# Performance work log

Hardware: AMD Instinct MI355X
Metric: run time of the kernel (lower is better)

## Reference

```python
import jax, jax.numpy as jnp
import numpy as np

CHUNK, STEP, NCHUNK = 75, 25, 22
DIM, HEADS = 64, 8
BN_EPS = 1e-5


def _conv1d(x, w, b):
    # x: [N, Cin, L], w: [Cout, Cin, K] (torch layout), VALID padding, stride 1
    y = jax.lax.conv_general_dilated(x, w, (1,), 'VALID',
                                     dimension_numbers=('NCH', 'OIH', 'NCH'))
    return y + b[None, :, None]


def _bn(x, gamma, beta, mean, var):
    # inference-mode batchnorm over channel dim of [N, C, L]
    scale = gamma / jnp.sqrt(var + BN_EPS)
    return (x - mean[None, :, None]) * scale[None, :, None] + beta[None, :, None]


def _swish(x):
    return x * jax.nn.sigmoid(x)


def _encode(audio, p):
    # audio: [B, 1, L] -> overlapping chunks [B, 22, 1, 75] via gather (unfold)
    B = audio.shape[0]
    idx = np.arange(NCHUNK)[:, None] * STEP + np.arange(CHUNK)[None, :]  # [22, 75]
    x = audio[:, :, idx]                      # [B, 1, 22, 75]
    x = x.transpose(0, 2, 1, 3).reshape(B * NCHUNK, 1, CHUNK)
    x = _swish(_bn(_conv1d(x, p['w1'], p['b1']), p['g1'], p['be1'], p['m1'], p['v1']))  # [B*22,16,50]
    x = _swish(_bn(_conv1d(x, p['w2'], p['b2']), p['g2'], p['be2'], p['m2'], p['v2']))  # [B*22,32,25]
    x = _swish(_bn(_conv1d(x, p['w3'], p['b3']), p['g3'], p['be3'], p['m3'], p['v3']))  # [B*22,64,1]
    return x[:, :, 0].reshape(B, NCHUNK, DIM)  # concat over chunks == seq of 22 tokens


def _mha(feat, p):
    # per-head full-width linears (torch Linear: y = x @ W.T + b), stacked over heads
    # Wq/Wk/Wv: [H, D, D]; bq/bk/bv: [H, D]
    B, S, D = feat.shape
    Q = jnp.einsum('bsd,hed->bhse', feat, p['Wq']) + p['bq'][None, :, None, :]
    K = jnp.einsum('bsd,hed->bhse', feat, p['Wk']) + p['bk'][None, :, None, :]
    V = jnp.einsum('bsd,hed->bhse', feat, p['Wv']) + p['bv'][None, :, None, :]
    A = jax.nn.softmax(jnp.einsum('bhse,bhte->bhst', Q, K), axis=-1)  # no 1/sqrt(d) scaling in source
    O = jnp.einsum('bhst,bhte->bhse', A, V)       # [B, H, S, D]
    O = O.transpose(0, 2, 1, 3).reshape(B, S, HEADS * D)  # concat heads along feature dim
    return O @ p['Wfc'].T + p['bfc']              # [B, S, D]


def setup_inputs() -> dict:
    key = jax.random.key(0)
    ks = jax.random.split(key, 16)
    B, L = 4096, 600
    C1, C2 = DIM // 4, DIM // 2
    inp = {
        'audio_vec1': jax.random.normal(ks[0], (B, 1, L), jnp.float32),
        'audio_vec2': jax.random.normal(ks[1], (B, 1, L), jnp.float32),
        # conv stack
        'w1': jax.random.normal(ks[2], (C1, 1, 26), jnp.float32) * 0.05,
        'b1': jnp.zeros((C1,), jnp.float32),
        'g1': jnp.ones((C1,), jnp.float32), 'be1': jnp.zeros((C1,), jnp.float32),
        'm1': jnp.zeros((C1,), jnp.float32), 'v1': jnp.ones((C1,), jnp.float32),
        'w2': jax.random.normal(ks[3], (C2, C1, 26), jnp.float32) * 0.05,
        'b2': jnp.zeros((C2,), jnp.float32),
        'g2': jnp.ones((C2,), jnp.float32), 'be2': jnp.zeros((C2,), jnp.float32),
        'm2': jnp.zeros((C2,), jnp.float32), 'v2': jnp.ones((C2,), jnp.float32),
        'w3': jax.random.normal(ks[4], (DIM, C2, 25), jnp.float32) * 0.05,
        'b3': jnp.zeros((DIM,), jnp.float32),
        'g3': jnp.ones((DIM,), jnp.float32), 'be3': jnp.zeros((DIM,), jnp.float32),
        'm3': jnp.zeros((DIM,), jnp.float32), 'v3': jnp.ones((DIM,), jnp.float32),
        # attention (per-head full-width projections)
        'Wq': jax.random.normal(ks[5], (HEADS, DIM, DIM), jnp.float32) * 0.05,
        'bq': jnp.zeros((HEADS, DIM), jnp.float32),
        'Wk': jax.random.normal(ks[6], (HEADS, DIM, DIM), jnp.float32) * 0.05,
        'bk': jnp.zeros((HEADS, DIM), jnp.float32),
        'Wv': jax.random.normal(ks[7], (HEADS, DIM, DIM), jnp.float32) * 0.05,
        'bv': jnp.zeros((HEADS, DIM), jnp.float32),
        'Wfc': jax.random.normal(ks[8], (DIM, HEADS * DIM), jnp.float32) * 0.05,
        'bfc': jnp.zeros((DIM,), jnp.float32),
        # final fc
        'Wout': jax.random.normal(ks[9], (DIM, DIM), jnp.float32) * 0.05,
        'bout': jnp.zeros((DIM,), jnp.float32),
    }
    return inp


def reference(audio_vec1, audio_vec2, w1, b1, g1, be1, m1, v1,
              w2, b2, g2, be2, m2, v2, w3, b3, g3, be3, m3, v3,
              Wq, bq, Wk, bk, Wv, bv, Wfc, bfc, Wout, bout):
    p = dict(w1=w1, b1=b1, g1=g1, be1=be1, m1=m1, v1=v1,
             w2=w2, b2=b2, g2=g2, be2=be2, m2=m2, v2=v2,
             w3=w3, b3=b3, g3=g3, be3=be3, m3=m3, v3=v3,
             Wq=Wq, bq=bq, Wk=Wk, bk=bk, Wv=Wv, bv=bv, Wfc=Wfc, bfc=bfc)
    f1 = _encode(audio_vec1, p)   # [B, 22, 64]
    f2 = _encode(audio_vec2, p)
    f1 = _mha(f1, p).mean(axis=1) @ Wout.T + bout  # [B, 64]
    f2 = _mha(f2, p).mean(axis=1) @ Wout.T + bout
    return (f1, f2)
```

## Files before the change

### kernel.cpp

```cpp
#include <hip/hip_runtime.h>
#include <math.h>

#define NCHUNK 22
#define SEQLEN 600
#define BN_EPS 1e-5f

#define OFF_W1F    0
#define OFF_W2F    1024
#define OFF_W3F    14336
#define OFF_MHF    65536
#define OFF_WC     98304
#define OFF_UH     131072
#define OFF_WH     131584
#define OFF_CH     132096
#define OFF_CBIAS  132104
#define OFF_WCOMB  132168
#define OFF_FEAT   164936
#define REPACK_N   132104

typedef short bf16x8 __attribute__((ext_vector_type(8)));
typedef float f32x4 __attribute__((ext_vector_type(4)));
typedef float f32x16 __attribute__((ext_vector_type(16)));

#if __has_builtin(__builtin_amdgcn_perm)
#define PERM_HI(r0, r1) __builtin_amdgcn_perm((r1), (r0), 0x05040100u)
#define PERM_LO(r0, r1) __builtin_amdgcn_perm((r1), (r0), 0x07060302u)
#else
#define PERM_HI(r0, r1) (((r0) & 0xFFFFu) | ((r1) << 16))
#define PERM_LO(r0, r1) (((r0) >> 16) | ((r1) & 0xFFFF0000u))
#endif

__device__ __forceinline__ float swishf(float z) {
    return z / (1.f + __expf(-z));
}
__device__ __forceinline__ unsigned short bf16_rne(float f) {
    unsigned int u = __float_as_uint(f);
    return (unsigned short)((u + 0x7FFFu + ((u >> 16) & 1u)) >> 16);
}
__device__ __forceinline__ float bf16_tof(unsigned short h) {
    return __uint_as_float(((unsigned int)h) << 16);
}
__device__ __forceinline__ unsigned int pack_hl(float f) {
    unsigned int u = __float_as_uint(f);
    unsigned int h = (u + 0x7FFFu + ((u >> 16) & 1u)) >> 16;
    float r = f - __uint_as_float(h << 16);
    unsigned int v = __float_as_uint(r);
    unsigned int l = (v + 0x7FFFu + ((v >> 16) & 1u)) >> 16;
    return h | (l << 16);
}
__device__ __forceinline__ unsigned int dup_word(float f, int pat) {
    unsigned short h = bf16_rne(f);
    unsigned short v = pat ? bf16_rne(f - bf16_tof(h)) : h;
    return (unsigned int)v | ((unsigned int)v << 16);
}
__device__ __forceinline__ unsigned int frag_word(float f0, float f1, int hl) {
    unsigned short h0 = bf16_rne(f0), h1 = bf16_rne(f1);
    if (hl == 0) return (unsigned int)h0 | ((unsigned int)h1 << 16);
    unsigned short l0 = bf16_rne(f0 - bf16_tof(h0));
    unsigned short l1 = bf16_rne(f1 - bf16_tof(h1));
    return (unsigned int)l0 | ((unsigned int)l1 << 16);
}
__device__ __forceinline__ void frag_from_packed(const unsigned int* p, bf16x8& h8, bf16x8& l8) {
    unsigned int r0 = p[0], r1 = p[1], r2 = p[2], r3 = p[3];
    unsigned int r4 = p[4], r5 = p[5], r6 = p[6], r7 = p[7];
    union U { unsigned int w[4]; bf16x8 v; } H, L;
    H.w[0] = PERM_HI(r0, r1); H.w[1] = PERM_HI(r2, r3);
    H.w[2] = PERM_HI(r4, r5); H.w[3] = PERM_HI(r6, r7);
    L.w[0] = PERM_LO(r0, r1); L.w[1] = PERM_LO(r2, r3);
    L.w[2] = PERM_LO(r4, r5); L.w[3] = PERM_LO(r6, r7);
    h8 = H.v; l8 = L.v;
}

__global__ __launch_bounds__(256) void repack_kernel(
    const float* __restrict__ w1, const float* __restrict__ w2, const float* __restrict__ w3,
    const float* __restrict__ Wq, const float* __restrict__ Wk, const float* __restrict__ Wv,
    const float* __restrict__ Wfc, const float* __restrict__ Wout,
    const float* __restrict__ bq, const float* __restrict__ bk,
    float* __restrict__ ws)
{
    int tid = blockIdx.x * 256 + threadIdx.x;
    unsigned int* wsu = (unsigned int*)ws;
    if (tid < 1024) {
        int r = tid & 3, lane = (tid >> 2) & 63, pat = (tid >> 8) & 1, ph = (tid >> 9) & 1;
        int li = lane & 15, lg = lane >> 4;
        int k = ph * 16 + lg * 4 + r;
        float f = (k < 26) ? w1[li * 26 + k] : 0.f;
        wsu[OFF_W1F + tid] = dup_word(f, pat);
    }
    int t2 = tid - 1024;
    if (t2 >= 0 && t2 < 13312) {
        int r = t2 & 3, lane = (t2 >> 2) & 63, hl = (t2 >> 8) & 1, s = t2 >> 9;
        int co = lane & 31;
        int ci0 = (lane >> 5) * 8;
        float f0 = w2[co * 416 + (ci0 + 2 * r) * 26 + s];
        float f1 = w2[co * 416 + (ci0 + 2 * r + 1) * 26 + s];
        wsu[OFF_W2F + t2] = frag_word(f0, f1, hl);
    }
    int t3 = tid - 14336;
    if (t3 >= 0 && t3 < 51200) {
        int r = t3 & 3, l = (t3 >> 2) & 63, hl = (t3 >> 8) & 1;
        int nt = (t3 >> 9) & 3, s = t3 >> 11;
        int co = nt * 16 + (l & 15);
        int k0 = s * 32 + (l >> 4) * 8 + 2 * r;
        float f0 = w3[co * 800 + (k0 & 31) * 25 + (k0 >> 5)];
        float f1 = w3[co * 800 + ((k0 + 1) & 31) * 25 + ((k0 + 1) >> 5)];
        wsu[OFF_W3F + t3] = frag_word(f0, f1, hl);
    }
    int t4 = tid - 65536;
    if (t4 >= 0 && t4 < 32768) {
        int r = t4 & 3, l = (t4 >> 2) & 63, hl = (t4 >> 8) & 1;
        int nt = (t4 >> 9) & 3, ks = (t4 >> 11) & 1, h = t4 >> 12;
        int n = nt * 16 + (l & 15);
        int d0 = ks * 32 + (l >> 4) * 8 + 2 * r;
        const float* wqh = Wq + h * 4096;
        const float* wkh = Wk + h * 4096;
        float f0 = 0.f, f1 = 0.f;
        #pragma unroll 8
        for (int e = 0; e < 64; ++e) {
            float wk_en = wkh[e * 64 + n];
            f0 = fmaf(wqh[e * 64 + d0],     wk_en, f0);
            f1 = fmaf(wqh[e * 64 + d0 + 1], wk_en, f1);
        }
        wsu[OFF_MHF + t4] = frag_word(f0, f1, hl);
    }
    int t7 = tid - 98304;
    if (t7 >= 0 && t7 < 32768) {
        int k = t7 & 63, j = t7 >> 6;
        float acc = 0.f;
        #pragma unroll 8
        for (int d = 0; d < 64; ++d)
            acc = fmaf(Wfc[d * 512 + j], Wout[k * 64 + d], acc);
        ws[OFF_WCOMB + t7] = acc;
    }
    int t8 = tid - 131072;
    if (t8 >= 0 && t8 < 512) {
        int h = t8 >> 6, d = t8 & 63;
        float acc = 0.f;
        #pragma unroll 8
        for (int e = 0; e < 64; ++e) acc = fmaf(Wq[h * 4096 + e * 64 + d], bk[h * 64 + e], acc);
        ws[OFF_UH + t8] = acc;
    }
    int t9 = tid - 131584;
    if (t9 >= 0 && t9 < 512) {
        int h = t9 >> 6, d = t9 & 63;
        float acc = 0.f;
        #pragma unroll 8
        for (int e = 0; e < 64; ++e) acc = fmaf(Wk[h * 4096 + e * 64 + d], bq[h * 64 + e], acc);
        ws[OFF_WH + t9] = acc;
    }
    int t10 = tid - 132096;
    if (t10 >= 0 && t10 < 8) {
        float acc = 0.f;
        #pragma unroll 8
        for (int e = 0; e < 64; ++e) acc = fmaf(bq[t10 * 64 + e], bk[t10 * 64 + e], acc);
        ws[OFF_CH + t10] = acc;
    }
}

__global__ __launch_bounds__(256) void repack2_kernel(
    const float* __restrict__ Wv, float* __restrict__ ws)
{
    int tid = blockIdx.x * 256 + threadIdx.x;
    int k = tid & 63, j = tid >> 6;
    int h = j >> 6, d = j & 63;
    const float* wcomb = ws + OFF_WCOMB + (size_t)(h * 64) * 64 + k;
    const float* wv = Wv + h * 4096 + d;
    float acc = 0.f;
    #pragma unroll 8
    for (int e = 0; e < 64; ++e)
        acc = fmaf(wv[e * 64], wcomb[e * 64], acc);
    ws[OFF_WC + tid] = acc;
}

__global__ __launch_bounds__(64) void cbias_kernel(
    const float* __restrict__ Wfc, const float* __restrict__ Wout,
    const float* __restrict__ bfc, const float* __restrict__ bout,
    const float* __restrict__ bv, float* __restrict__ ws)
{
    __shared__ float sd_s[64];
    int t = threadIdx.x;
    float acc = 0.f;
    for (int j = 0; j < 512; ++j) acc = fmaf(bv[j], Wfc[t * 512 + j], acc);
    sd_s[t] = acc;
    __syncthreads();
    float cb = bout[t];
    #pragma unroll 8
    for (int dp = 0; dp < 64; ++dp) cb = fmaf(bfc[dp] + sd_s[dp], Wout[t * 64 + dp], cb);
    ws[OFF_CBIAS + t] = cb;
}

__global__ __launch_bounds__(256, 6) void encoder_kernel(
    const float* __restrict__ audio1, const float* __restrict__ audio2,
    const float* __restrict__ b1, const float* __restrict__ g1, const float* __restrict__ be1,
    const float* __restrict__ m1, const float* __restrict__ v1,
    const float* __restrict__ b2, const float* __restrict__ g2, const float* __restrict__ be2,
    const float* __restrict__ m2, const float* __restrict__ v2,
    const float* __restrict__ b3, const float* __restrict__ g3, const float* __restrict__ be3,
    const float* __restrict__ m3, const float* __restrict__ v3,
    float* __restrict__ ws, int B)
{
    __shared__ __align__(16) unsigned int smem[4456];
    unsigned int* a_p = smem;
    unsigned short* y1h16 = (unsigned short*)(smem + 192);
    unsigned short* y1l16 = (unsigned short*)(smem + 1732);
    unsigned short* y2h16 = (unsigned short*)(smem + 192);
    unsigned short* y2l16 = (unsigned short*)(smem + 2212);
    float* A_s  = (float*)(smem + 4232);
    float* Bc_s = (float*)(smem + 4344);

    int t = threadIdx.x;
    int blk = blockIdx.x;
    int seq = blk / 5, tile = blk - seq * 5;
    int tc = (tile == 4) ? 2 : 5;
    int nq = 25 * tc;
    int ny1 = nq + 25;
    int na = nq + 50;
    const unsigned int* wsu = (const unsigned int*)ws;
    int lane = t & 63, wid = t >> 6;
    int li = lane & 15, lg = lane >> 4;

    const float* audio = (seq < B ? audio1 + (size_t)seq * SEQLEN
                                  : audio2 + (size_t)(seq - B) * SEQLEN) + tile * 125;
    uint4 w1b[2][2];
    #pragma unroll
    for (int ph = 0; ph < 2; ++ph)
        #pragma unroll
        for (int pat = 0; pat < 2; ++pat)
            w1b[ph][pat] = *(const uint4*)(wsu + OFF_W1F + ((ph * 2 + pat) * 64 + lane) * 4);

    if (t < 192) a_p[t] = (t < na) ? pack_hl(audio[t]) : 0u;
    if (t < 16)       { float A = g1[t] * rsqrtf(v1[t] + BN_EPS); A_s[t] = A; Bc_s[t] = (b1[t] - m1[t]) * A + be1[t]; }
    else if (t < 48)  { int i = t - 16; float A = g2[i] * rsqrtf(v2[i] + BN_EPS); A_s[t] = A; Bc_s[t] = (b2[i] - m2[i]) * A + be2[i]; }
    else if (t < 112) { int i = t - 48; float A = g3[i] * rsqrtf(v3[i] + BN_EPS); A_s[t] = A; Bc_s[t] = (b3[i] - m3[i]) * A + be3[i]; }
    for (int i = ny1 * 10 + t; i < 1540; i += 256) {
        (smem + 192)[i] = 0u;
        (smem + 1732)[i] = 0u;
    }
    __syncthreads();

    {
        int nMt1 = (ny1 + 15) >> 4;
        float Ai = A_s[li], Bi = Bc_s[li];
        for (int mt = wid; mt < nMt1; mt += 4) {
            f32x4 acc = {0.f, 0.f, 0.f, 0.f};
            #pragma unroll
            for (int ph = 0; ph < 2; ++ph) {
                const unsigned int* ap = a_p + mt * 16 + li + ph * 16 + lg * 4;
                union { unsigned int w[4]; bf16x8 v; } A;
                A.w[0] = ap[0]; A.w[1] = ap[1]; A.w[2] = ap[2]; A.w[3] = ap[3];
                bf16x8 b0 = *(const bf16x8*)&w1b[ph][0];
                bf16x8 b1 = *(const bf16x8*)&w1b[ph][1];
                acc = __builtin_amdgcn_mfma_f32_16x16x32_bf16(A.v, b0, acc, 0, 0, 0);
                acc = __builtin_amdgcn_mfma_f32_16x16x32_bf16(A.v, b1, acc, 0, 0, 0);
            }
            #pragma unroll
            for (int r = 0; r < 4; ++r) {
                int p = mt * 16 + lg * 4 + r;
                if (p < ny1) {
                    float f = swishf(fmaf(acc[r], Ai, Bi));
                    unsigned short hh = bf16_rne(f);
                    unsigned short ll = bf16_rne(f - bf16_tof(hh));
                    y1h16[p * 20 + li] = hh;
                    y1l16[p * 20 + li] = ll;
                }
            }
        }
    }
    __syncthreads();

    int row0 = wid * 32 + (lane & 31);
    int ci0 = (lane >> 5) * 8;
    f32x16 acc2;
    #pragma unroll
    for (int r = 0; r < 16; ++r) acc2[r] = 0.f;
    {
        const uint4* w2f4 = (const uint4*)(wsu + OFF_W2F);
        uint4 nbh0 = w2f4[(0 * 2 + 0) * 64 + lane];
        uint4 nbl0 = w2f4[(0 * 2 + 1) * 64 + lane];
        uint4 nbh1 = w2f4[(1 * 2 + 0) * 64 + lane];
        uint4 nbl1 = w2f4[(1 * 2 + 1) * 64 + lane];
        for (int stg = 0; stg < 13; ++stg) {
            uint4 cbh0 = nbh0, cbl0 = nbl0, cbh1 = nbh1, cbl1 = nbl1;
            if (stg < 12) {
                int s2 = stg * 2 + 2, s3 = stg * 2 + 3;
                nbh0 = w2f4[(s2 * 2 + 0) * 64 + lane];
                nbl0 = w2f4[(s2 * 2 + 1) * 64 + lane];
                nbh1 = w2f4[(s3 * 2 + 0) * 64 + lane];
                nbl1 = w2f4[(s3 * 2 + 1) * 64 + lane];
            }
            #pragma unroll
            for (int half = 0; half < 2; ++half) {
                int s = stg * 2 + half;
                bf16x8 bh = *(const bf16x8*)(half ? &cbh1 : &cbh0);
                bf16x8 bl = *(const bf16x8*)(half ? &cbl1 : &cbl0);
                const unsigned short* hp = y1h16 + (row0 + s) * 20 + ci0;
                const unsigned short* lp = y1l16 + (row0 + s) * 20 + ci0;
                union { uint2 u[2]; bf16x8 v; } Ah, Al;
                Ah.u[0] = *(const uint2*)hp; Ah.u[1] = *(const uint2*)(hp + 4);
                Al.u[0] = *(const uint2*)lp; Al.u[1] = *(const uint2*)(lp + 4);
                acc2 = __builtin_amdgcn_mfma_f32_32x32x16_bf16(Ah.v, bh, acc2, 0, 0, 0);
                acc2 = __builtin_amdgcn_mfma_f32_32x32x16_bf16(Al.v, bh, acc2, 0, 0, 0);
                acc2 = __builtin_amdgcn_mfma_f32_32x32x16_bf16(Ah.v, bl, acc2, 0, 0, 0);
            }
        }
    }
    __syncthreads();
    {
        int co = lane & 31;
        float Ac = A_s[16 + co], Bc = Bc_s[16 + co];
        int rbase = 4 * (lane >> 5) + wid * 32;
        #pragma unroll
        for (int reg = 0; reg < 16; ++reg) {
            int q = rbase + (reg & 3) + 8 * (reg >> 2);
            if (q < nq) {
                int cc = q / 25, qp = q - cc * 25;
                float f = swishf(fmaf(acc2[reg], Ac, Bc));
                unsigned short hh = bf16_rne(f);
                unsigned short ll = bf16_rne(f - bf16_tof(hh));
                y2h16[cc * 808 + qp * 32 + co] = hh;
                y2l16[cc * 808 + qp * 32 + co] = ll;
            }
        }
    }
    __syncthreads();

    {
        const uint4* w3f4 = (const uint4*)(wsu + OFF_W3F);
        f32x4 acc3 = {0.f, 0.f, 0.f, 0.f};
        for (int b5 = 0; b5 < 5; ++b5) {
            uint4 BH[5], BL[5];
            #pragma unroll
            for (int i = 0; i < 5; ++i) {
                int s = b5 * 5 + i;
                BH[i] = w3f4[((s * 4 + wid) * 2 + 0) * 64 + lane];
                BL[i] = w3f4[((s * 4 + wid) * 2 + 1) * 64 + lane];
            }
            #pragma unroll
            for (int i = 0; i < 5; ++i) {
                int s = b5 * 5 + i;
                bf16x8 ah = {}, al = {};
                if (li < tc) {
                    ah = *(const bf16x8*)(y2h16 + li * 808 + s * 32 + lg * 8);
                    al = *(const bf16x8*)(y2l16 + li * 808 + s * 32 + lg * 8);
                }
                bf16x8 bh = *(const bf16x8*)&BH[i];
                bf16x8 bl = *(const bf16x8*)&BL[i];
                acc3 = __builtin_amdgcn_mfma_f32_16x16x32_bf16(ah, bh, acc3, 0, 0, 0);
                acc3 = __builtin_amdgcn_mfma_f32_16x16x32_bf16(al, bh, acc3, 0, 0, 0);
                acc3 = __builtin_amdgcn_mfma_f32_16x16x32_bf16(ah, bl, acc3, 0, 0, 0);
            }
        }
        int co = wid * 16 + li;
        float A3 = A_s[48 + co], B3 = Bc_s[48 + co];
        unsigned int* featp = (unsigned int*)ws + OFF_FEAT;
        #pragma unroll
        for (int r = 0; r < 4; ++r) {
            int cc = lg * 4 + r;
            if (cc < tc)
                featp[((size_t)(seq * NCHUNK + tile * 5 + cc)) * 64 + co]
                    = pack_hl(swishf(fmaf(acc3[r], A3, B3)));
        }
    }
}

__global__ __launch_bounds__(256, 3) void mha_kernel(
    const float* __restrict__ ws, float* __restrict__ out, int B)
{
    __shared__ __align__(16) unsigned int smem[12398];
    unsigned int* f_p = smem;
    float* f32F   = (float*)(smem + 7480);
    float* rowqc  = (float*)(smem + 10942);
    float* wh_s   = (float*)(smem + 11118);
    float* fbar_s = (float*)(smem + 11630);
    float* fred   = (float*)(smem + 12142);

    int t = threadIdx.x, b = blockIdx.x;
    int lane = t & 63, wid = t >> 6;
    int li = lane & 15, lg = lane >> 4;
    const unsigned int* wsu = (const unsigned int*)ws;
    const unsigned int* featp = wsu + OFF_FEAT + (size_t)b * 1408;
    for (int i = t; i < 1408; i += 256) {
        unsigned int w = featp[i];
        int s = i >> 6, d = i & 63;
        f_p[s * 68 + d] = w;
        f32F[s * 65 + d] = __uint_as_float(w << 16) + __uint_as_float(w & 0xFFFF0000u);
    }
    for (int i = t; i < 512; i += 256) wh_s[i] = ws[OFF_WH + i];
    __syncthreads();

    unsigned short* qh_w = (unsigned short*)(smem + 1496 + wid * 1496);
    unsigned short* ql_w = qh_w + 1496;
    float* P      = (float*)(smem + 8910) + wid * 484;
    float* abar_w = (float*)(smem + 10846) + wid * 24;
    float* rowq_w = rowqc + wid * 44;

    if (lane < 44) {
        int hl = lane / 22, s = lane - hl * 22;
        int h = wid * 2 + hl;
        float acc = ws[OFF_CH + h];
        const float* uh = ws + OFF_UH + h * 64;
        #pragma unroll 8
        for (int d = 0; d < 64; ++d) acc = fmaf(f32F[s * 65 + d], uh[d], acc);
        rowq_w[lane] = acc;
    }

    bf16x8 fah[2][2], fal[2][2];
    #pragma unroll
    for (int mt = 0; mt < 2; ++mt)
        #pragma unroll
        for (int ks = 0; ks < 2; ++ks)
            frag_from_packed(f_p + (mt * 16 + li) * 68 + ks * 32 + lg * 8,
                             fah[mt][ks], fal[mt][ks]);

    const uint4* mhf4 = (const uint4*)(wsu + OFF_MHF);

    #pragma unroll
    for (int hh = 0; hh < 2; ++hh) {
        int h = wid * 2 + hh;
        f32x4 a0t0 = {0,0,0,0}, a0t1 = a0t0, a0t2 = a0t0, a0t3 = a0t0;
        f32x4 a1t0 = a0t0, a1t1 = a0t0, a1t2 = a0t0, a1t3 = a0t0;
        #pragma unroll
        for (int nt = 0; nt < 4; ++nt) {
            f32x4 r0 = {0,0,0,0}, r1 = {0,0,0,0};
            #pragma unroll
            for (int ks = 0; ks < 2; ++ks) {
                uint4 bh4 = mhf4[h * 1024 + ks * 512 + nt * 128 + lane];
                uint4 bl4 = mhf4[h * 1024 + ks * 512 + nt * 128 + 64 + lane];
                bf16x8 bh = *(const bf16x8*)&bh4;
                bf16x8 bl = *(const bf16x8*)&bl4;
                r0 = __builtin_amdgcn_mfma_f32_16x16x32_bf16(fah[0][ks], bh, r0, 0, 0, 0);
                r0 = __builtin_amdgcn_mfma_f32_16x16x32_bf16(fal[0][ks], bh, r0, 0, 0, 0);
                r0 = __builtin_amdgcn_mfma_f32_16x16x32_bf16(fah[0][ks], bl, r0, 0, 0, 0);
                r1 = __builtin_amdgcn_mfma_f32_16x16x32_bf16(fah[1][ks], bh, r1, 0, 0, 0);
                r1 = __builtin_amdgcn_mfma_f32_16x16x32_bf16(fal[1][ks], bh, r1, 0, 0, 0);
                r1 = __builtin_amdgcn_mfma_f32_16x16x32_bf16(fah[1][ks], bl, r1, 0, 0, 0);
            }
            if (nt == 0) { a0t0 = r0; a1t0 = r1; }
            else if (nt == 1) { a0t1 = r0; a1t1 = r1; }
            else if (nt == 2) { a0t2 = r0; a1t2 = r1; }
            else { a0t3 = r0; a1t3 = r1; }
        }
        #pragma unroll
        for (int nt = 0; nt < 4; ++nt) {
            int col = nt * 16 + li;
            float wv = wh_s[h * 64 + col];
            f32x4 r0 = (nt == 0) ? a0t0 : (nt == 1) ? a0t1 : (nt == 2) ? a0t2 : a0t3;
            f32x4 r1 = (nt == 0) ? a1t0 : (nt == 1) ? a1t1 : (nt == 2) ? a1t2 : a1t3;
            #pragma unroll
            for (int r = 0; r < 4; ++r) {
                int row0 = lg * 4 + r;
                float v0 = r0[r] + wv;
                unsigned short h0 = bf16_rne(v0);
                qh_w[row0 * 68 + col] = h0;
                ql_w[row0 * 68 + col] = bf16_rne(v0 - bf16_tof(h0));
                int row1 = 16 + row0;
                if (row1 < 22) {
                    float v1 = r1[r] + wv;
                    unsigned short h1 = bf16_rne(v1);
                    qh_w[row1 * 68 + col] = h1;
                    ql_w[row1 * 68 + col] = bf16_rne(v1 - bf16_tof(h1));
                }
            }
        }
        #pragma unroll
        for (int mt = 0; mt < 2; ++mt) {
            union { uint2 u[2]; bf16x8 v; } Th0, Tl0, Th1, Tl1;
            {
                const unsigned short* hp = qh_w + (mt * 16 + li) * 68 + lg * 8;
                const unsigned short* lp = ql_w + (mt * 16 + li) * 68 + lg * 8;
                Th0.u[0] = *(const uint2*)hp;        Th0.u[1] = *(const uint2*)(hp + 4);
                Tl0.u[0] = *(const uint2*)lp;        Tl0.u[1] = *(const uint2*)(lp + 4);
                Th1.u[0] = *(const uint2*)(hp + 32); Th1.u[1] = *(const uint2*)(hp + 36);
                Tl1.u[0] = *(const uint2*)(lp + 32); Tl1.u[1] = *(const uint2*)(lp + 36);
            }
            #pragma unroll
            for (int ntile = 0; ntile < 2; ++ntile) {
                f32x4 sacc = {0, 0, 0, 0};
                sacc = __builtin_amdgcn_mfma_f32_16x16x32_bf16(Th0.v, fah[ntile][0], sacc, 0, 0, 0);
                sacc = __builtin_amdgcn_mfma_f32_16x16x32_bf16(Tl0.v, fah[ntile][0], sacc, 0, 0, 0);
                sacc = __builtin_amdgcn_mfma_f32_16x16x32_bf16(Th0.v, fal[ntile][0], sacc, 0, 0, 0);
                sacc = __builtin_amdgcn_mfma_f32_16x16x32_bf16(Th1.v, fah[ntile][1], sacc, 0, 0, 0);
                sacc = __builtin_amdgcn_mfma_f32_16x16x32_bf16(Tl1.v, fah[ntile][1], sacc, 0, 0, 0);
                sacc = __builtin_amdgcn_mfma_f32_16x16x32_bf16(Th1.v, fal[ntile][1], sacc, 0, 0, 0);
                int u = ntile * 16 + li;
                #pragma unroll
                for (int r = 0; r < 4; ++r) {
                    int s = mt * 16 + lg * 4 + r;
                    if (s < 22 && u < 22)
                        P[s * 22 + u] = sacc[r] + rowq_w[hh * 22 + s];
                }
            }
        }
        {
            int r2 = lane >> 1, c2 = lane & 1;
            float pm = -1e30f, psum = 0.f;
            if (lane < 44) {
                #pragma unroll
                for (int j = 0; j < 11; ++j) pm = fmaxf(pm, P[r2 * 22 + c2 * 11 + j]);
            }
            float m = fmaxf(__shfl(pm, 2 * lane), __shfl(pm, 2 * lane + 1));
            float rm = __shfl(m, r2);
            if (lane < 44) {
                #pragma unroll
                for (int j = 0; j < 11; ++j) {
                    int idx = r2 * 22 + c2 * 11 + j;
                    float ev = __expf(P[idx] - rm);
                    P[idx] = ev;
                    psum += ev;
                }
            }
            float sum = __shfl(psum, 2 * lane) + __shfl(psum, 2 * lane + 1);
            if (lane < 22) abar_w[lane] = 1.f / sum;
            if (lane < 22) {
                float a = 0.f;
                #pragma unroll
                for (int s = 0; s < 22; ++s) a += P[s * 22 + lane] * abar_w[s];
                abar_w[lane] = a * (1.f / 22.f);
            }
            float acc = 0.f;
            #pragma unroll
            for (int u = 0; u < 22; ++u) acc = fmaf(abar_w[u], f32F[u * 65 + lane], acc);
            fbar_s[h * 64 + lane] = acc;
        }
    }
    __syncthreads();
    {
        int d = t & 63, part = t >> 6;
        const float* wc = ws + OFF_WC;
        float acc = 0.f;
        for (int j = part * 128; j < part * 128 + 128; ++j)
            acc = fmaf(fbar_s[j], wc[j * 64 + d], acc);
        fred[part * 64 + d] = acc;
    }
    __syncthreads();
    if (t < 64)
        out[(size_t)b * 64 + t] = ws[OFF_CBIAS + t]
            + fred[t] + fred[64 + t] + fred[128 + t] + fred[192 + t];
}

extern "C" void kernel_launch(void* const* d_in, const int* in_sizes, int n_in,
                              void* d_out, int out_size, void* d_ws, size_t ws_size,
                              hipStream_t stream) {
    const float* audio1 = (const float*)d_in[0];
    const float* audio2 = (const float*)d_in[1];
    const float* w1   = (const float*)d_in[2];
    const float* b1   = (const float*)d_in[3];
    const float* g1   = (const float*)d_in[4];
    const float* be1  = (const float*)d_in[5];
    const float* m1   = (const float*)d_in[6];
    const float* v1   = (const float*)d_in[7];
    const float* w2   = (const float*)d_in[8];
    const float* b2   = (const float*)d_in[9];
    const float* g2   = (const float*)d_in[10];
    const float* be2  = (const float*)d_in[11];
    const float* m2   = (const float*)d_in[12];
    const float* v2   = (const float*)d_in[13];
    const float* w3   = (const float*)d_in[14];
    const float* b3   = (const float*)d_in[15];
    const float* g3   = (const float*)d_in[16];
    const float* be3  = (const float*)d_in[17];
    const float* m3   = (const float*)d_in[18];
    const float* v3   = (const float*)d_in[19];
    const float* Wq   = (const float*)d_in[20];
    const float* bq   = (const float*)d_in[21];
    const float* Wk   = (const float*)d_in[22];
    const float* bk   = (const float*)d_in[23];
    const float* Wv   = (const float*)d_in[24];
    const float* bv   = (const float*)d_in[25];
    const float* Wfc  = (const float*)d_in[26];
    const float* bfc  = (const float*)d_in[27];
    const float* Wout = (const float*)d_in[28];
    const float* bout = (const float*)d_in[29];

    float* ws  = (float*)d_ws;
    float* out = (float*)d_out;
    int B = in_sizes[0] / SEQLEN;
    int nseq = 2 * B;

    repack_kernel<<<(REPACK_N + 255) / 256, 256, 0, stream>>>(
        w1, w2, w3, Wq, Wk, Wv, Wfc, Wout, bq, bk, ws);
    repack2_kernel<<<128, 256, 0, stream>>>(Wv, ws);
    cbias_kernel<<<1, 64, 0, stream>>>(Wfc, Wout, bfc, bout, bv, ws);
    encoder_kernel<<<nseq * 5, 256, 0, stream>>>(audio1, audio2,
        b1, g1, be1, m1, v1,
        b2, g2, be2, m2, v2,
        b3, g3, be3, m3, v3,
        ws, B);
    mha_kernel<<<nseq, 256, 0, stream>>>(ws, out, B);
}
```

Baseline: 888.6 us.

## Process two encoder tiles per block, sharing conv2 weights via LDS double-buffering

```diff
diff --git a/kernel.cpp b/kernel.cpp
--- a/kernel.cpp
+++ b/kernel.cpp
@@ -189,7 +189,7 @@
     ws[OFF_CBIAS + t] = cb;
 }
 
-__global__ __launch_bounds__(256, 6) void encoder_kernel(
+__global__ __launch_bounds__(256, 4) void encoder_kernel(
     const float* __restrict__ audio1, const float* __restrict__ audio2,
     const float* __restrict__ b1, const float* __restrict__ g1, const float* __restrict__ be1,
     const float* __restrict__ m1, const float* __restrict__ v1,
@@ -199,28 +199,38 @@
     const float* __restrict__ m3, const float* __restrict__ v3,
     float* __restrict__ ws, int B)
 {
-    __shared__ __align__(16) unsigned int smem[4456];
-    unsigned int* a_p = smem;
-    unsigned short* y1h16 = (unsigned short*)(smem + 192);
-    unsigned short* y1l16 = (unsigned short*)(smem + 1732);
-    unsigned short* y2h16 = (unsigned short*)(smem + 192);
-    unsigned short* y2l16 = (unsigned short*)(smem + 2212);
-    float* A_s  = (float*)(smem + 4232);
-    float* Bc_s = (float*)(smem + 4344);
+    __shared__ __align__(16) unsigned int smem[8816];
+    unsigned int* a_p0 = smem;
+    unsigned int* a_p1 = smem + 192;
+    unsigned int* w2f  = smem + 384;
+    unsigned short* y1h0 = (unsigned short*)(smem + 2432);
+    unsigned short* y1l0 = (unsigned short*)(smem + 3972);
+    unsigned short* y1h1 = (unsigned short*)(smem + 5512);
+    unsigned short* y1l1 = (unsigned short*)(smem + 7052);
+    unsigned short* y2h0 = (unsigned short*)(smem + 384);
+    unsigned short* y2l0 = (unsigned short*)(smem + 2404);
+    unsigned short* y2h1 = (unsigned short*)(smem + 4424);
+    unsigned short* y2l1 = (unsigned short*)(smem + 6444);
+    float* A_s  = (float*)(smem + 8592);
+    float* Bc_s = (float*)(smem + 8704);
 
     int t = threadIdx.x;
     int blk = blockIdx.x;
-    int seq = blk / 5, tile = blk - seq * 5;
-    int tc = (tile == 4) ? 2 : 5;
-    int nq = 25 * tc;
-    int ny1 = nq + 25;
-    int na = nq + 50;
+    int g0 = blk * 2, g1v = g0 + 1;
+    int seq0 = g0 / 5, tile0 = g0 - seq0 * 5;
+    int seq1 = g1v / 5, tile1 = g1v - seq1 * 5;
+    int tc0 = (tile0 == 4) ? 2 : 5, tc1 = (tile1 == 4) ? 2 : 5;
+    int nq0 = 25 * tc0, nq1 = 25 * tc1;
+    int ny10 = nq0 + 25, ny11 = nq1 + 25;
+    int na0 = nq0 + 50, na1 = nq1 + 50;
     const unsigned int* wsu = (const unsigned int*)ws;
     int lane = t & 63, wid = t >> 6;
     int li = lane & 15, lg = lane >> 4;
 
-    const float* audio = (seq < B ? audio1 + (size_t)seq * SEQLEN
-                                  : audio2 + (size_t)(seq - B) * SEQLEN) + tile * 125;
+    const float* aud0 = (seq0 < B ? audio1 + (size_t)seq0 * SEQLEN
+                                  : audio2 + (size_t)(seq0 - B) * SEQLEN) + tile0 * 125;
+    const float* aud1 = (seq1 < B ? audio1 + (size_t)seq1 * SEQLEN
+                                  : audio2 + (size_t)(seq1 - B) * SEQLEN) + tile1 * 125;
     uint4 w1b[2][2];
     #pragma unroll
     for (int ph = 0; ph < 2; ++ph)
@@ -228,40 +238,55 @@
         for (int pat = 0; pat < 2; ++pat)
             w1b[ph][pat] = *(const uint4*)(wsu + OFF_W1F + ((ph * 2 + pat) * 64 + lane) * 4);
 
-    if (t < 192) a_p[t] = (t < na) ? pack_hl(audio[t]) : 0u;
+    if (t < 192) {
+        a_p0[t] = (t < na0) ? pack_hl(aud0[t]) : 0u;
+        a_p1[t] = (t < na1) ? pack_hl(aud1[t]) : 0u;
+    }
+    *(uint4*)(w2f + t * 4) = *(const uint4*)(wsu + OFF_W2F + t * 4);
     if (t < 16)       { float A = g1[t] * rsqrtf(v1[t] + BN_EPS); A_s[t] = A; Bc_s[t] = (b1[t] - m1[t]) * A + be1[t]; }
     else if (t < 48)  { int i = t - 16; float A = g2[i] * rsqrtf(v2[i] + BN_EPS); A_s[t] = A; Bc_s[t] = (b2[i] - m2[i]) * A + be2[i]; }
     else if (t < 112) { int i = t - 48; float A = g3[i] * rsqrtf(v3[i] + BN_EPS); A_s[t] = A; Bc_s[t] = (b3[i] - m3[i]) * A + be3[i]; }
-    for (int i = ny1 * 10 + t; i < 1540; i += 256) {
-        (smem + 192)[i] = 0u;
-        (smem + 1732)[i] = 0u;
+    for (int i = ny10 * 10 + t; i < 1540; i += 256) {
+        (smem + 2432)[i] = 0u;
+        (smem + 3972)[i] = 0u;
+    }
+    for (int i = ny11 * 10 + t; i < 1540; i += 256) {
+        (smem + 5512)[i] = 0u;
+        (smem + 7052)[i] = 0u;
     }
     __syncthreads();
 
     {
-        int nMt1 = (ny1 + 15) >> 4;
         float Ai = A_s[li], Bi = Bc_s[li];
-        for (int mt = wid; mt < nMt1; mt += 4) {
-            f32x4 acc = {0.f, 0.f, 0.f, 0.f};
-            #pragma unroll
-            for (int ph = 0; ph < 2; ++ph) {
-                const unsigned int* ap = a_p + mt * 16 + li + ph * 16 + lg * 4;
-                union { unsigned int w[4]; bf16x8 v; } A;
-                A.w[0] = ap[0]; A.w[1] = ap[1]; A.w[2] = ap[2]; A.w[3] = ap[3];
-                bf16x8 b0 = *(const bf16x8*)&w1b[ph][0];
-                bf16x8 b1 = *(const bf16x8*)&w1b[ph][1];
-                acc = __builtin_amdgcn_mfma_f32_16x16x32_bf16(A.v, b0, acc, 0, 0, 0);
-                acc = __builtin_amdgcn_mfma_f32_16x16x32_bf16(A.v, b1, acc, 0, 0, 0);
-            }
-            #pragma unroll
-            for (int r = 0; r < 4; ++r) {
-                int p = mt * 16 + lg * 4 + r;
-                if (p < ny1) {
-                    float f = swishf(fmaf(acc[r], Ai, Bi));
-                    unsigned short hh = bf16_rne(f);
-                    unsigned short ll = bf16_rne(f - bf16_tof(hh));
-                    y1h16[p * 20 + li] = hh;
-                    y1l16[p * 20 + li] = ll;
+        #pragma unroll
+        for (int tl = 0; tl < 2; ++tl) {
+            const unsigned int* ap_base = tl ? a_p1 : a_p0;
+            unsigned short* yh = tl ? y1h1 : y1h0;
+            unsigned short* yl = tl ? y1l1 : y1l0;
+            int ny1 = tl ? ny11 : ny10;
+            int nMt1 = (ny1 + 15) >> 4;
+            for (int mt = wid; mt < nMt1; mt += 4) {
+                f32x4 acc = {0.f, 0.f, 0.f, 0.f};
+                #pragma unroll
+                for (int ph = 0; ph < 2; ++ph) {
+                    const unsigned int* ap = ap_base + mt * 16 + li + ph * 16 + lg * 4;
+                    union { unsigned int w[4]; bf16x8 v; } A;
+                    A.w[0] = ap[0]; A.w[1] = ap[1]; A.w[2] = ap[2]; A.w[3] = ap[3];
+                    bf16x8 b0 = *(const bf16x8*)&w1b[ph][0];
+                    bf16x8 b1 = *(const bf16x8*)&w1b[ph][1];
+                    acc = __builtin_amdgcn_mfma_f32_16x16x32_bf16(A.v, b0, acc, 0, 0, 0);
+                    acc = __builtin_amdgcn_mfma_f32_16x16x32_bf16(A.v, b1, acc, 0, 0, 0);
+                }
+                #pragma unroll
+                for (int r = 0; r < 4; ++r) {
+                    int p = mt * 16 + lg * 4 + r;
+                    if (p < ny1) {
+                        float f = swishf(fmaf(acc[r], Ai, Bi));
+                        unsigned short hh = bf16_rne(f);
+                        unsigned short ll = bf16_rne(f - bf16_tof(hh));
+                        yh[p * 20 + li] = hh;
+                        yl[p * 20 + li] = ll;
+                    }
                 }
             }
         }
@@ -270,41 +295,45 @@
 
     int row0 = wid * 32 + (lane & 31);
     int ci0 = (lane >> 5) * 8;
-    f32x16 acc2;
+    f32x16 accA, accB;
     #pragma unroll
-    for (int r = 0; r < 16; ++r) acc2[r] = 0.f;
-    {
-        const uint4* w2f4 = (const uint4*)(wsu + OFF_W2F);
-        uint4 nbh0 = w2f4[(0 * 2 + 0) * 64 + lane];
-        uint4 nbl0 = w2f4[(0 * 2 + 1) * 64 + lane];
-        uint4 nbh1 = w2f4[(1 * 2 + 0) * 64 + lane];
-        uint4 nbl1 = w2f4[(1 * 2 + 1) * 64 + lane];
-        for (int stg = 0; stg < 13; ++stg) {
-            uint4 cbh0 = nbh0, cbl0 = nbl0, cbh1 = nbh1, cbl1 = nbl1;
-            if (stg < 12) {
-                int s2 = stg * 2 + 2, s3 = stg * 2 + 3;
-                nbh0 = w2f4[(s2 * 2 + 0) * 64 + lane];
-                nbl0 = w2f4[(s2 * 2 + 1) * 64 + lane];
-                nbh1 = w2f4[(s3 * 2 + 0) * 64 + lane];
-                nbl1 = w2f4[(s3 * 2 + 1) * 64 + lane];
-            }
-            #pragma unroll
-            for (int half = 0; half < 2; ++half) {
-                int s = stg * 2 + half;
-                bf16x8 bh = *(const bf16x8*)(half ? &cbh1 : &cbh0);
-                bf16x8 bl = *(const bf16x8*)(half ? &cbl1 : &cbl0);
-                const unsigned short* hp = y1h16 + (row0 + s) * 20 + ci0;
-                const unsigned short* lp = y1l16 + (row0 + s) * 20 + ci0;
+    for (int r = 0; r < 16; ++r) { accA[r] = 0.f; accB[r] = 0.f; }
+
+    for (int stg = 0; stg < 13; ++stg) {
+        uint4 vnext;
+        if (stg < 12)
+            vnext = *(const uint4*)(wsu + OFF_W2F + (stg + 1) * 1024 + t * 4);
+        const unsigned int* cur = w2f + (stg & 1) * 1024;
+        #pragma unroll
+        for (int half = 0; half < 2; ++half) {
+            int s = stg * 2 + half;
+            bf16x8 bh = *(const bf16x8*)(cur + half * 512 + lane * 4);
+            bf16x8 bl = *(const bf16x8*)(cur + half * 512 + 256 + lane * 4);
+            {
+                const unsigned short* hp = y1h0 + (row0 + s) * 20 + ci0;
+                const unsigned short* lp = y1l0 + (row0 + s) * 20 + ci0;
                 union { uint2 u[2]; bf16x8 v; } Ah, Al;
                 Ah.u[0] = *(const uint2*)hp; Ah.u[1] = *(const uint2*)(hp + 4);
                 Al.u[0] = *(const uint2*)lp; Al.u[1] = *(const uint2*)(lp + 4);
-                acc2 = __builtin_amdgcn_mfma_f32_32x32x16_bf16(Ah.v, bh, acc2, 0, 0, 0);
-                acc2 = __builtin_amdgcn_mfma_f32_32x32x16_bf16(Al.v, bh, acc2, 0, 0, 0);
-                acc2 = __builtin_amdgcn_mfma_f32_32x32x16_bf16(Ah.v, bl, acc2, 0, 0, 0);
-            }
-        }
-    }
-    __syncthreads();
+                accA = __builtin_amdgcn_mfma_f32_32x32x16_bf16(Ah.v, bh, accA, 0, 0, 0);
+                accA = __builtin_amdgcn_mfma_f32_32x32x16_bf16(Al.v, bh, accA, 0, 0, 0);
+                accA = __builtin_amdgcn_mfma_f32_32x32x16_bf16(Ah.v, bl, accA, 0, 0, 0);
+            }
+            {
+                const unsigned short* hp = y1h1 + (row0 + s) * 20 + ci0;
+                const unsigned short* lp = y1l1 + (row0 + s) * 20 + ci0;
+                union { uint2 u[2]; bf16x8 v; } Ah, Al;
+                Ah.u[0] = *(const uint2*)hp; Ah.u[1] = *(const uint2*)(hp + 4);
+                Al.u[0] = *(const uint2*)lp; Al.u[1] = *(const uint2*)(lp + 4);
+                accB = __builtin_amdgcn_mfma_f32_32x32x16_bf16(Ah.v, bh, accB, 0, 0, 0);
+                accB = __builtin_amdgcn_mfma_f32_32x32x16_bf16(Al.v, bh, accB, 0, 0, 0);
+                accB = __builtin_amdgcn_mfma_f32_32x32x16_bf16(Ah.v, bl, accB, 0, 0, 0);
+            }
+        }
+        if (stg < 12)
+            *(uint4*)(w2f + ((stg + 1) & 1) * 1024 + t * 4) = vnext;
+        __syncthreads();
+    }
     {
         int co = lane & 31;
         float Ac = A_s[16 + co], Bc = Bc_s[16 + co];
@@ -312,13 +341,21 @@
         #pragma unroll
         for (int reg = 0; reg < 16; ++reg) {
             int q = rbase + (reg & 3) + 8 * (reg >> 2);
-            if (q < nq) {
+            if (q < nq0) {
                 int cc = q / 25, qp = q - cc * 25;
-                float f = swishf(fmaf(acc2[reg], Ac, Bc));
+                float f = swishf(fmaf(accA[reg], Ac, Bc));
                 unsigned short hh = bf16_rne(f);
                 unsigned short ll = bf16_rne(f - bf16_tof(hh));
-                y2h16[cc * 808 + qp * 32 + co] = hh;
-                y2l16[cc * 808 + qp * 32 + co] = ll;
+                y2h0[cc * 808 + qp * 32 + co] = hh;
+                y2l0[cc * 808 + qp * 32 + co] = ll;
+            }
+            if (q < nq1) {
+                int cc = q / 25, qp = q - cc * 25;
+                float f = swishf(fmaf(accB[reg], Ac, Bc));
+                unsigned short hh = bf16_rne(f);
+                unsigned short ll = bf16_rne(f - bf16_tof(hh));
+                y2h1[cc * 808 + qp * 32 + co] = hh;
+                y2l1[cc * 808 + qp * 32 + co] = ll;
             }
         }
     }
@@ -339,9 +376,17 @@
             for (int i = 0; i < 5; ++i) {
                 int s = b5 * 5 + i;
                 bf16x8 ah = {}, al = {};
-                if (li < tc) {
-                    ah = *(const bf16x8*)(y2h16 + li * 808 + s * 32 + lg * 8);
-                    al = *(const bf16x8*)(y2l16 + li * 808 + s * 32 + lg * 8);
+                if (li < 5) {
+                    if (li < tc0) {
+                        ah = *(const bf16x8*)(y2h0 + li * 808 + s * 32 + lg * 8);
+                        al = *(const bf16x8*)(y2l0 + li * 808 + s * 32 + lg * 8);
+                    }
+                } else if (li < 10) {
+                    int c = li - 5;
+                    if (c < tc1) {
+                        ah = *(const bf16x8*)(y2h1 + c * 808 + s * 32 + lg * 8);
+                        al = *(const bf16x8*)(y2l1 + c * 808 + s * 32 + lg * 8);
+                    }
                 }
                 bf16x8 bh = *(const bf16x8*)&BH[i];
                 bf16x8 bl = *(const bf16x8*)&BL[i];
@@ -356,9 +401,16 @@
         #pragma unroll
         for (int r = 0; r < 4; ++r) {
             int cc = lg * 4 + r;
-            if (cc < tc)
-                featp[((size_t)(seq * NCHUNK + tile * 5 + cc)) * 64 + co]
-                    = pack_hl(swishf(fmaf(acc3[r], A3, B3)));
+            if (cc < 5) {
+                if (cc < tc0)
+                    featp[((size_t)(seq0 * NCHUNK + tile0 * 5 + cc)) * 64 + co]
+                        = pack_hl(swishf(fmaf(acc3[r], A3, B3)));
+            } else if (cc < 10) {
+                int c = cc - 5;
+                if (c < tc1)
+                    featp[((size_t)(seq1 * NCHUNK + tile1 * 5 + c)) * 64 + co]
+                        = pack_hl(swishf(fmaf(acc3[r], A3, B3)));
+            }
         }
     }
 }
@@ -576,12 +628,13 @@
     float* out = (float*)d_out;
     int B = in_sizes[0] / SEQLEN;
     int nseq = 2 * B;
+    int npair = nseq * 5 / 2;
 
     repack_kernel<<<(REPACK_N + 255) / 256, 256, 0, stream>>>(
         w1, w2, w3, Wq, Wk, Wv, Wfc, Wout, bq, bk, ws);
     repack2_kernel<<<128, 256, 0, stream>>>(Wv, ws);
     cbias_kernel<<<1, 64, 0, stream>>>(Wfc, Wout, bfc, bout, bv, ws);
-    encoder_kernel<<<nseq * 5, 256, 0, stream>>>(audio1, audio2,
+    encoder_kernel<<<npair, 256, 0, stream>>>(audio1, audio2,
         b1, g1, be1, m1, v1,
         b2, g2, be2, m2, v2,
         b3, g3, be3, m3, v3,
```

New measurement: 765.7 us. -13.8%, faster.
